# Performance work log

Measured on AMD Instinct MI355X. Metric: run time of the kernel, lower is better.

Reference implementation:

```python
import jax, jax.numpy as jnp
import numpy as np

NUM_CLASSES = 27
ALPHABET = 21

def _build_table():
    # Precomputed 27x21 lookup table equivalent to one_hot + slice + B/Z/J fixups.
    t = np.zeros((NUM_CLASSES, ALPHABET), dtype=np.float32)
    for c in range(1, 22):          # codes 1..21: standard amino acids
        t[c, c - 1] = 1.0
    t[22, 2] = 0.5; t[22, 11] = 0.5  # B = 0.5 D + 0.5 N
    t[23, 3] = 0.5; t[23, 13] = 0.5  # Z = 0.5 E + 0.5 Q
    t[24, 7] = 0.5; t[24, 9] = 0.5   # J = 0.5 I + 0.5 L
    # codes 0 (pad), 25 (U), 26 (O) stay all-zero, matching the torch slicing.
    return jnp.asarray(t)

def setup_inputs() -> dict:
    key = jax.random.key(0)
    sequence = jax.random.randint(key, (512, 2048), 0, NUM_CLASSES, dtype=jnp.int64)
    table = _build_table()
    return {"sequence": sequence, "table": table}

def reference(sequence, table):
    # Single gather: [B, L] int codes -> [B, L, 21] float encoding.
    return table[sequence]
```

## Files before the change

### kernel.cpp

```cpp
#include <hip/hip_runtime.h>


constexpr int NUM_CLASSES = 27;
constexpr int ALPHABET    = 21;
constexpr int TABLE_ELEMS = NUM_CLASSES * ALPHABET;

__global__ __launch_bounds__(256) void pseudo_onehot_kernel(
    const int* __restrict__ seq,
    const float* __restrict__ table,
    float* __restrict__ out,
    int n_vec4,
    int total)
{
    __shared__ float t[TABLE_ELEMS];
    for (int i = threadIdx.x; i < TABLE_ELEMS; i += 256)
        t[i] = table[i];
    __syncthreads();

    const int tid     = blockIdx.x * 256 + threadIdx.x;
    const int nthread = gridDim.x * 256;

    for (int g = tid; g < n_vec4; g += nthread) {
        const int base = g * 4;
        float v[4];
#pragma unroll
        for (int j = 0; j < 4; ++j) {
            const int idx  = base + j;
            const int e    = idx / ALPHABET;
            const int c    = idx - e * ALPHABET;
            const int code = seq[e];
            v[j] = t[code * ALPHABET + c];
        }
        float4 o = make_float4(v[0], v[1], v[2], v[3]);
        *reinterpret_cast<float4*>(out + base) = o;
    }

    for (int idx = n_vec4 * 4 + tid; idx < total; idx += nthread) {
        const int e = idx / ALPHABET;
        const int c = idx - e * ALPHABET;
        out[idx] = t[seq[e] * ALPHABET + c];
    }
}

extern "C" void kernel_launch(void* const* d_in, const int* in_sizes, int n_in,
                              void* d_out, int out_size, void* d_ws, size_t ws_size,
                              hipStream_t stream) {
    const int*   seq   = (const int*)d_in[0];
    const float* table = (const float*)d_in[1];
    float*       out   = (float*)d_out;

    const int n_vec4 = out_size / 4;
    const int block  = 256;
    int grid = (n_vec4 + block - 1) / block;
    if (grid > 2048) grid = 2048;

    pseudo_onehot_kernel<<<grid, block, 0, stream>>>(seq, table, out,
                                                     n_vec4, out_size);
}
```

Measured before the change: 21.22 us.

## Stage premultiplied codes per block in LDS and drop grid-stride loop

Each block now handles a fixed tile of 1024 sequence elements, loading their codes once with vector loads and storing code*21 in shared memory. Output float4s are assembled from at most two staged codes, which replaces per-float divisions and repeated global loads of the sequence. This reduces ALU and load-issue overhead in a store-bound kernel. The tail path assumes the output size is a multiple of four, and the grid is no longer capped.

Result: faster. 19.81 us (-6.6%).

```diff
diff --git a/kernel.cpp b/kernel.cpp
--- a/kernel.cpp
+++ b/kernel.cpp
@@ -1,44 +1,69 @@
 #include <hip/hip_runtime.h>
 
 
-constexpr int NUM_CLASSES = 27;
-constexpr int ALPHABET    = 21;
-constexpr int TABLE_ELEMS = NUM_CLASSES * ALPHABET;
+constexpr int ALPHABET         = 21;
+constexpr int TABLE_ELEMS      = 27 * 21;
+constexpr int BLOCK            = 256;
+constexpr int ELEMS_PER_BLOCK  = 1024;
+constexpr int FLOATS_PER_BLOCK = ELEMS_PER_BLOCK * ALPHABET;
+constexpr int ITERS            = FLOATS_PER_BLOCK / 4 / BLOCK;
 
 __global__ __launch_bounds__(256) void pseudo_onehot_kernel(
     const int* __restrict__ seq,
     const float* __restrict__ table,
     float* __restrict__ out,
-    int n_vec4,
-    int total)
+    int n_elems,
+    long n_floats)
 {
     __shared__ float t[TABLE_ELEMS];
-    for (int i = threadIdx.x; i < TABLE_ELEMS; i += 256)
+    __shared__ int   codes21[ELEMS_PER_BLOCK + 4];
+
+    for (int i = threadIdx.x; i < TABLE_ELEMS; i += BLOCK)
         t[i] = table[i];
+
+    const int eBase = blockIdx.x * ELEMS_PER_BLOCK;
+    {
+        const int i = threadIdx.x;
+        const int e = eBase + i * 4;
+        int4 c4;
+        if (e + 3 < n_elems) {
+            c4 = *reinterpret_cast<const int4*>(seq + e);
+        } else {
+            c4.x = (e + 0 < n_elems) ? seq[e + 0] : 0;
+            c4.y = (e + 1 < n_elems) ? seq[e + 1] : 0;
+            c4.z = (e + 2 < n_elems) ? seq[e + 2] : 0;
+            c4.w = (e + 3 < n_elems) ? seq[e + 3] : 0;
+        }
+        c4.x *= ALPHABET; c4.y *= ALPHABET; c4.z *= ALPHABET; c4.w *= ALPHABET;
+        *reinterpret_cast<int4*>(&codes21[i * 4]) = c4;
+        if (i == 0) {
+            codes21[ELEMS_PER_BLOCK]     = 0;
+            codes21[ELEMS_PER_BLOCK + 1] = 0;
+        }
+    }
     __syncthreads();
 
-    const int tid     = blockIdx.x * 256 + threadIdx.x;
-    const int nthread = gridDim.x * 256;
+    const long blockFloatBase = (long)blockIdx.x * FLOATS_PER_BLOCK;
 
-    for (int g = tid; g < n_vec4; g += nthread) {
-        const int base = g * 4;
-        float v[4];
 #pragma unroll
-        for (int j = 0; j < 4; ++j) {
-            const int idx  = base + j;
-            const int e    = idx / ALPHABET;
-            const int c    = idx - e * ALPHABET;
-            const int code = seq[e];
-            v[j] = t[code * ALPHABET + c];
-        }
-        float4 o = make_float4(v[0], v[1], v[2], v[3]);
-        *reinterpret_cast<float4*>(out + base) = o;
-    }
+    for (int j = 0; j < ITERS; ++j) {
+        const int  f  = threadIdx.x + j * BLOCK;
+        const int  lf = f * 4;
+        const long gf = blockFloatBase + lf;
+        if (gf + 3 >= n_floats) break;
 
-    for (int idx = n_vec4 * 4 + tid; idx < total; idx += nthread) {
-        const int e = idx / ALPHABET;
-        const int c = idx - e * ALPHABET;
-        out[idx] = t[seq[e] * ALPHABET + c];
+        const int le = lf / ALPHABET;
+        const int lc = lf - le * ALPHABET;
+        const int A  = codes21[le] + lc;
+        const int B  = codes21[le + 1] + lc - ALPHABET;
+
+        float4 o;
+        o.x = t[(lc + 0 < ALPHABET) ? A + 0 : B + 0];
+        o.y = t[(lc + 1 < ALPHABET) ? A + 1 : B + 1];
+        o.z = t[(lc + 2 < ALPHABET) ? A + 2 : B + 2];
+        o.w = t[(lc + 3 < ALPHABET) ? A + 3 : B + 3];
+
+        *reinterpret_cast<float4*>(out + gf) = o;
     }
 }
 
@@ -49,11 +74,9 @@
     const float* table = (const float*)d_in[1];
     float*       out   = (float*)d_out;
 
-    const int n_vec4 = out_size / 4;
-    const int block  = 256;
-    int grid = (n_vec4 + block - 1) / block;
-    if (grid > 2048) grid = 2048;
+    const int n_elems = in_sizes[0];
+    const int grid    = (n_elems + ELEMS_PER_BLOCK - 1) / ELEMS_PER_BLOCK;
 
-    pseudo_onehot_kernel<<<grid, block, 0, stream>>>(seq, table, out,
-                                                     n_vec4, out_size);
+    pseudo_onehot_kernel<<<grid, BLOCK, 0, stream>>>(seq, table, out,
+                                                     n_elems, (long)out_size);
 }
```
